# Optimization experiments

Measured on AMD Instinct MI355X. Metric: run time of the kernel, lower is better.

## Reference

```python
import jax, jax.numpy as jnp
import numpy as np

HEADS = 4
HEAD_DIM = 32
NEG_SLOPE = 0.2  # PyG GATConv default

N_NODES = 100000
N_EDGES = 1600000
IN_CH = 128
N_GRAPHS = 64


def setup_inputs() -> dict:
    key = jax.random.key(0)
    ks = jax.random.split(key, 6)
    x = jax.random.normal(ks[0], (N_NODES, IN_CH), dtype=jnp.float32)
    edge_index = jax.random.randint(ks[1], (2, N_EDGES), 0, N_NODES, dtype=jnp.int32)
    batch = jnp.sort(jax.random.randint(ks[2], (N_NODES,), 0, N_GRAPHS, dtype=jnp.int32))
    # glorot-style scaling
    W = jax.random.normal(ks[3], (IN_CH, HEADS * HEAD_DIM), dtype=jnp.float32) * (1.0 / np.sqrt(IN_CH))
    att_src = jax.random.normal(ks[4], (HEADS, HEAD_DIM), dtype=jnp.float32) * (1.0 / np.sqrt(HEAD_DIM))
    att_dst = jax.random.normal(ks[5], (HEADS, HEAD_DIM), dtype=jnp.float32) * (1.0 / np.sqrt(HEAD_DIM))
    bias = jnp.zeros((HEADS * HEAD_DIM,), dtype=jnp.float32)
    return {"x": x, "edge_index": edge_index, "batch": batch,
            "W": W, "att_src": att_src, "att_dst": att_dst, "bias": bias}


def reference(x, edge_index, batch, W, att_src, att_dst, bias):
    # batch is unused (collect_embeddings=False path); kept for signature fidelity
    N = x.shape[0]
    # add self-loops (PyG GATConv default add_self_loops=True)
    loop = jnp.arange(N, dtype=edge_index.dtype)
    src = jnp.concatenate([edge_index[0], loop])  # [E+N]
    dst = jnp.concatenate([edge_index[1], loop])  # [E+N]

    # linear transform, split heads: [N, H, C]
    xt = (x @ W).reshape(N, HEADS, HEAD_DIM)
    a_src = jnp.einsum('nhc,hc->nh', xt, att_src)  # [N, H]
    a_dst = jnp.einsum('nhc,hc->nh', xt, att_dst)  # [N, H]

    # edge-wise attention logits with LeakyReLU
    alpha = a_src[src] + a_dst[dst]                # [E+N, H]
    alpha = jnp.where(alpha >= 0, alpha, NEG_SLOPE * alpha)

    # segment softmax over incoming edges of each destination node
    seg_max = jax.ops.segment_max(alpha, dst, num_segments=N)   # [N, H]
    alpha = jnp.exp(alpha - seg_max[dst])
    seg_sum = jax.ops.segment_sum(alpha, dst, num_segments=N)   # [N, H]
    alpha = alpha / (seg_sum[dst] + 1e-16)

    # weighted scatter-aggregate of source features
    msg = xt[src] * alpha[:, :, None]                            # [E+N, H, C]
    out = jax.ops.segment_sum(msg, dst, num_segments=N)          # [N, H, C]
    out = out.reshape(N, HEADS * HEAD_DIM) + bias                # concat heads
    return jax.nn.relu(out)
```

## Files before the change

### kernel.cpp

```cpp
#include <hip/hip_runtime.h>
#include <hip/hip_bf16.h>

#define HEADS 4
#define CH 128
#define NTILE 9
#define NCOLS (NTILE*16)
#define WSTRIDE 136
#define CAP 64

typedef __attribute__((ext_vector_type(8))) short short8v;
typedef __attribute__((ext_vector_type(4))) float f32x4;

static __device__ __forceinline__ unsigned short f2bf(float f) {
    __hip_bfloat16 b = __float2bfloat16(f);
    return *reinterpret_cast<unsigned short*>(&b);
}
static __device__ __forceinline__ float bf2f(unsigned short u) {
    unsigned int x = ((unsigned int)u) << 16;
    return __uint_as_float(x);
}

__global__ __launch_bounds__(256) void k_prep(
    const float* __restrict__ W, const float* __restrict__ att_src,
    const float* __restrict__ att_dst, unsigned short* __restrict__ Wt)
{
    int idx = blockIdx.x * 256 + threadIdx.x;
    if (idx >= NCOLS * WSTRIDE) return;
    int c = idx / WSTRIDE;
    int k = idx % WSTRIDE;
    float v = 0.f;
    if (k < CH) {
        if (c < CH) {
            v = W[(size_t)k * CH + c];
        } else if (c < CH + 8) {
            int q = c - CH;
            const float* att = (q < 4) ? att_src : att_dst;
            int h = q & 3;
            float s = 0.f;
            #pragma unroll
            for (int t = 0; t < 32; ++t)
                s += W[(size_t)k * CH + h * 32 + t] * att[h * 32 + t];
            v = s;
        }
    }
    Wt[idx] = f2bf(v);
}

__global__ __launch_bounds__(256, 4) void k_fused(
    const float* __restrict__ x, const unsigned short* __restrict__ Wt,
    unsigned short* __restrict__ xt, float* __restrict__ a_src, float* __restrict__ a_dst,
    int N, const int* __restrict__ ei, int E,
    int* __restrict__ cursor, int* __restrict__ csr, int gemmBlocks, int scatB)
{
    __shared__ unsigned short Wl[NCOLS * WSTRIDE];
    const int tid = threadIdx.x;

    if ((int)blockIdx.x >= gemmBlocks) {
        int b     = blockIdx.x - gemmBlocks;
        int slice = b & 7;
        int c     = b >> 3;
        int B     = scatB >> 3;
        int lo = (int)((long long)N * slice / 8);
        int hi = (int)((long long)N * (slice + 1) / 8);
        for (int i = c * 256 + tid; i < E; i += B * 256) {
            int dst = ei[E + i];
            if (dst >= lo && dst < hi) {
                int pos = atomicAdd(&cursor[dst], 1);
                if (pos < CAP) csr[((size_t)dst << 6) + pos] = ei[i];
            }
        }
        return;
    }

    {
        const float4* s4 = (const float4*)Wt;
        float4* d4 = (float4*)Wl;
        for (int i = tid; i < NCOLS * WSTRIDE * 2 / 16; i += 256)
            d4[i] = s4[i];
    }
    __syncthreads();

    const int wv = tid >> 6;
    const int l  = tid & 63;
    const int la = l & 15;
    const int lb = l >> 4;

    const int r = blockIdx.x * 64 + wv * 16 + la;

    float4 f[4][2];
    if (r < N) {
        const float4* p = (const float4*)(x + (size_t)r * CH);
        #pragma unroll
        for (int ks = 0; ks < 4; ++ks) {
            f[ks][0] = p[ks * 8 + lb * 2];
            f[ks][1] = p[ks * 8 + lb * 2 + 1];
        }
    } else {
        #pragma unroll
        for (int ks = 0; ks < 4; ++ks)
            f[ks][0] = f[ks][1] = make_float4(0.f, 0.f, 0.f, 0.f);
    }

    union U8 { short8v v; unsigned short u[8]; };
    short8v a[4];
    #pragma unroll
    for (int ks = 0; ks < 4; ++ks) {
        U8 ua;
        ua.u[0] = f2bf(f[ks][0].x); ua.u[1] = f2bf(f[ks][0].y);
        ua.u[2] = f2bf(f[ks][0].z); ua.u[3] = f2bf(f[ks][0].w);
        ua.u[4] = f2bf(f[ks][1].x); ua.u[5] = f2bf(f[ks][1].y);
        ua.u[6] = f2bf(f[ks][1].z); ua.u[7] = f2bf(f[ks][1].w);
        a[ks] = ua.v;
    }

    f32x4 acc[NTILE];
    #pragma unroll
    for (int n = 0; n < NTILE; ++n) acc[n] = (f32x4){0.f, 0.f, 0.f, 0.f};

    #pragma unroll
    for (int ks = 0; ks < 4; ++ks) {
        #pragma unroll
        for (int n = 0; n < NTILE; ++n) {
            short8v b = *(const short8v*)&Wl[(n * 16 + la) * WSTRIDE + ks * 32 + lb * 8];
            acc[n] = __builtin_amdgcn_mfma_f32_16x16x32_bf16(a[ks], b, acc[n], 0, 0, 0);
        }
    }

    const int rbase = blockIdx.x * 64 + wv * 16 + lb * 4;
    #pragma unroll
    for (int reg = 0; reg < 4; ++reg) {
        int gr = rbase + reg;
        if (gr >= N) continue;
        #pragma unroll
        for (int n = 0; n < 8; ++n)
            xt[(size_t)gr * CH + n * 16 + la] = f2bf(acc[n][reg]);
        if (la < 4)       a_src[(size_t)gr * 4 + la]       = acc[8][reg];
        else if (la < 8)  a_dst[(size_t)gr * 4 + (la - 4)] = acc[8][reg];
    }
}

__global__ __launch_bounds__(256) void k_gather(
    const int* __restrict__ cursor, const int* __restrict__ csr,
    const float* __restrict__ a_src, const float* __restrict__ a_dst,
    const unsigned short* __restrict__ xt, const float* __restrict__ bias,
    float* __restrict__ out, int N)
{
    int n = blockIdx.x * 4 + (threadIdx.x >> 6);
    if (n >= N) return;
    int l   = threadIdx.x & 63;
    int grp = l >> 4;
    int q   = l & 15;
    int h   = q >> 2;

    float ad = a_dst[(size_t)n * 4 + h];
    int cnt = cursor[n];
    if (cnt > CAP) cnt = CAP;
    const size_t base = (size_t)n << 6;

    float acc[8] = {0.f,0.f,0.f,0.f,0.f,0.f,0.f,0.f};
    float wsum = 0.f;
    for (int k = grp; k < cnt; k += 4) {
        int src = csr[base + k];
        float as = a_src[(size_t)src * 4 + h];
        float lg = as + ad;
        lg = (lg >= 0.f) ? lg : 0.2f * lg;
        float w = __expf(lg);
        wsum += w;
        float4 raw = ((const float4*)xt)[(size_t)src * 16 + q];
        union { float4 f; unsigned short u[8]; } uu; uu.f = raw;
        #pragma unroll
        for (int j = 0; j < 8; ++j) acc[j] += w * bf2f(uu.u[j]);
    }
    if (grp == 0) {
        float as = a_src[(size_t)n * 4 + h];
        float lg = as + ad;
        lg = (lg >= 0.f) ? lg : 0.2f * lg;
        float w = __expf(lg);
        wsum += w;
        float4 raw = ((const float4*)xt)[(size_t)n * 16 + q];
        union { float4 f; unsigned short u[8]; } uu; uu.f = raw;
        #pragma unroll
        for (int j = 0; j < 8; ++j) acc[j] += w * bf2f(uu.u[j]);
    }

    #pragma unroll
    for (int j = 0; j < 8; ++j) {
        acc[j] += __shfl_xor(acc[j], 16, 64);
        acc[j] += __shfl_xor(acc[j], 32, 64);
    }
    wsum += __shfl_xor(wsum, 16, 64);
    wsum += __shfl_xor(wsum, 32, 64);

    if (grp == 0) {
        float inv = 1.0f / wsum;
        float4 b0 = ((const float4*)bias)[q * 2];
        float4 b1 = ((const float4*)bias)[q * 2 + 1];
        float4 v0, v1;
        v0.x = fmaxf(fmaf(acc[0], inv, b0.x), 0.f);
        v0.y = fmaxf(fmaf(acc[1], inv, b0.y), 0.f);
        v0.z = fmaxf(fmaf(acc[2], inv, b0.z), 0.f);
        v0.w = fmaxf(fmaf(acc[3], inv, b0.w), 0.f);
        v1.x = fmaxf(fmaf(acc[4], inv, b1.x), 0.f);
        v1.y = fmaxf(fmaf(acc[5], inv, b1.y), 0.f);
        v1.z = fmaxf(fmaf(acc[6], inv, b1.z), 0.f);
        v1.w = fmaxf(fmaf(acc[7], inv, b1.w), 0.f);
        ((float4*)out)[(size_t)n * 32 + q * 2]     = v0;
        ((float4*)out)[(size_t)n * 32 + q * 2 + 1] = v1;
    }
}

extern "C" void kernel_launch(void* const* d_in, const int* in_sizes, int n_in,
                              void* d_out, int out_size, void* d_ws, size_t ws_size,
                              hipStream_t stream) {
    const float* x       = (const float*)d_in[0];
    const int*   ei      = (const int*)d_in[1];
    const float* W       = (const float*)d_in[3];
    const float* att_src = (const float*)d_in[4];
    const float* att_dst = (const float*)d_in[5];
    const float* bias    = (const float*)d_in[6];

    const int N = in_sizes[0] / CH;
    const int E = in_sizes[1] / 2;
    float* out = (float*)d_out;

    char* ws = (char*)d_ws;
    size_t p = 0;
    unsigned short* Wt = (unsigned short*)(ws + p); p += (size_t)NCOLS * WSTRIDE * 2;
    unsigned short* xt = (unsigned short*)(ws + p); p += (size_t)N * CH * 2;
    float* a_src  = (float*)(ws + p); p += (size_t)N * 4 * 4;
    float* a_dst  = (float*)(ws + p); p += (size_t)N * 4 * 4;
    int*   cursor = (int*)(ws + p);   p += (size_t)N * 4;
    int*   csr    = (int*)(ws + p);   p += (size_t)N * CAP * 4;

    hipMemsetAsync(cursor, 0, (size_t)N * 4, stream);

    k_prep<<<(NCOLS * WSTRIDE + 255) / 256, 256, 0, stream>>>(W, att_src, att_dst, Wt);

    const int gemmBlocks = (N + 63) / 64;
    const int scatB      = 1024;
    k_fused<<<gemmBlocks + scatB, 256, 0, stream>>>(x, Wt, xt, a_src, a_dst,
                                                    N, ei, E, cursor, csr,
                                                    gemmBlocks, scatB);

    k_gather<<<(N + 3) / 4, 256, 0, stream>>>(cursor, csr, a_src, a_dst,
                                              xt, bias, out, N);
}
```

Measured before the change: 181.5 us.

## Split fused scatter/GEMM kernel; stage x through swizzled LDS and coalesce xt stores

Separates the CSR scatter and the GEMM into two kernels, so the scatter no longer shares a launch with the GEMM and now runs 2048 blocks instead of 1024. The GEMM no longer copies the weight matrix into LDS; it reads B fragments directly from global memory, which is small enough to be served from cache. It loads and converts x into a swizzled LDS tile with coalesced reads, and stages the output through LDS so xt is written as full-row float4 stores instead of scattered 2-byte stores. This gives up concurrent execution of the two phases and relies on cache hits for the weight reads, in exchange for lower LDS use and higher occupancy.

```diff
diff --git a/kernel.cpp b/kernel.cpp
--- a/kernel.cpp
+++ b/kernel.cpp
@@ -46,37 +46,31 @@
     Wt[idx] = f2bf(v);
 }
 
-__global__ __launch_bounds__(256, 4) void k_fused(
+__global__ __launch_bounds__(256, 6) void k_gemm(
     const float* __restrict__ x, const unsigned short* __restrict__ Wt,
     unsigned short* __restrict__ xt, float* __restrict__ a_src, float* __restrict__ a_dst,
-    int N, const int* __restrict__ ei, int E,
-    int* __restrict__ cursor, int* __restrict__ csr, int gemmBlocks, int scatB)
-{
-    __shared__ unsigned short Wl[NCOLS * WSTRIDE];
+    int N)
+{
+    __shared__ unsigned short xl[64 * CH];
+    char* xb = (char*)xl;
     const int tid = threadIdx.x;
-
-    if ((int)blockIdx.x >= gemmBlocks) {
-        int b     = blockIdx.x - gemmBlocks;
-        int slice = b & 7;
-        int c     = b >> 3;
-        int B     = scatB >> 3;
-        int lo = (int)((long long)N * slice / 8);
-        int hi = (int)((long long)N * (slice + 1) / 8);
-        for (int i = c * 256 + tid; i < E; i += B * 256) {
-            int dst = ei[E + i];
-            if (dst >= lo && dst < hi) {
-                int pos = atomicAdd(&cursor[dst], 1);
-                if (pos < CAP) csr[((size_t)dst << 6) + pos] = ei[i];
-            }
-        }
-        return;
-    }
+    const int blk = blockIdx.x;
 
     {
-        const float4* s4 = (const float4*)Wt;
-        float4* d4 = (float4*)Wl;
-        for (int i = tid; i < NCOLS * WSTRIDE * 2 / 16; i += 256)
-            d4[i] = s4[i];
+        const float4* x4 = (const float4*)x;
+        #pragma unroll
+        for (int it = 0; it < 8; ++it) {
+            int i   = tid + it * 256;
+            int row = i >> 5, c4 = i & 31;
+            int gr  = blk * 64 + row;
+            float4 v = make_float4(0.f, 0.f, 0.f, 0.f);
+            if (gr < N) v = x4[(size_t)gr * 32 + c4];
+            ushort4 u;
+            u.x = f2bf(v.x); u.y = f2bf(v.y); u.z = f2bf(v.z); u.w = f2bf(v.w);
+            int byte = (row << 8) + (c4 << 3);
+            byte ^= (row & 15) << 4;
+            *(ushort4*)(xb + byte) = u;
+        }
     }
     __syncthreads();
 
@@ -84,34 +78,16 @@
     const int l  = tid & 63;
     const int la = l & 15;
     const int lb = l >> 4;
-
-    const int r = blockIdx.x * 64 + wv * 16 + la;
-
-    float4 f[4][2];
-    if (r < N) {
-        const float4* p = (const float4*)(x + (size_t)r * CH);
-        #pragma unroll
-        for (int ks = 0; ks < 4; ++ks) {
-            f[ks][0] = p[ks * 8 + lb * 2];
-            f[ks][1] = p[ks * 8 + lb * 2 + 1];
-        }
-    } else {
-        #pragma unroll
-        for (int ks = 0; ks < 4; ++ks)
-            f[ks][0] = f[ks][1] = make_float4(0.f, 0.f, 0.f, 0.f);
-    }
-
-    union U8 { short8v v; unsigned short u[8]; };
+    const int row = wv * 16 + la;
+
     short8v a[4];
     #pragma unroll
     for (int ks = 0; ks < 4; ++ks) {
-        U8 ua;
-        ua.u[0] = f2bf(f[ks][0].x); ua.u[1] = f2bf(f[ks][0].y);
-        ua.u[2] = f2bf(f[ks][0].z); ua.u[3] = f2bf(f[ks][0].w);
-        ua.u[4] = f2bf(f[ks][1].x); ua.u[5] = f2bf(f[ks][1].y);
-        ua.u[6] = f2bf(f[ks][1].z); ua.u[7] = f2bf(f[ks][1].w);
-        a[ks] = ua.v;
-    }
+        int byte = (row << 8) + (ks << 6) + (lb << 4);
+        byte ^= la << 4;
+        a[ks] = *(const short8v*)(xb + byte);
+    }
+    __syncthreads();
 
     f32x4 acc[NTILE];
     #pragma unroll
@@ -121,21 +97,67 @@
     for (int ks = 0; ks < 4; ++ks) {
         #pragma unroll
         for (int n = 0; n < NTILE; ++n) {
-            short8v b = *(const short8v*)&Wl[(n * 16 + la) * WSTRIDE + ks * 32 + lb * 8];
-            acc[n] = __builtin_amdgcn_mfma_f32_16x16x32_bf16(a[ks], b, acc[n], 0, 0, 0);
-        }
-    }
-
-    const int rbase = blockIdx.x * 64 + wv * 16 + lb * 4;
+            short8v bb = *(const short8v*)&Wt[(size_t)(n * 16 + la) * WSTRIDE + ks * 32 + lb * 8];
+            acc[n] = __builtin_amdgcn_mfma_f32_16x16x32_bf16(a[ks], bb, acc[n], 0, 0, 0);
+        }
+    }
+
     #pragma unroll
     for (int reg = 0; reg < 4; ++reg) {
-        int gr = rbase + reg;
-        if (gr >= N) continue;
-        #pragma unroll
-        for (int n = 0; n < 8; ++n)
-            xt[(size_t)gr * CH + n * 16 + la] = f2bf(acc[n][reg]);
-        if (la < 4)       a_src[(size_t)gr * 4 + la]       = acc[8][reg];
-        else if (la < 8)  a_dst[(size_t)gr * 4 + (la - 4)] = acc[8][reg];
+        int r = wv * 16 + lb * 4 + reg;
+        int swz = (r & 15) << 4;
+        #pragma unroll
+        for (int n = 0; n < 8; ++n) {
+            int byte = (r << 8) + ((n * 16 + la) << 1);
+            *(unsigned short*)(xb + (byte ^ swz)) = f2bf(acc[n][reg]);
+        }
+    }
+    __syncthreads();
+
+    {
+        #pragma unroll
+        for (int it = 0; it < 4; ++it) {
+            int j   = tid + it * 256;
+            int r   = j >> 4, g = j & 15;
+            int gr  = blk * 64 + r;
+            if (gr < N) {
+                int byte = (r << 8) + (g << 4);
+                byte ^= (r & 15) << 4;
+                float4 v = *(const float4*)(xb + byte);
+                ((float4*)xt)[(size_t)gr * 16 + g] = v;
+            }
+        }
+    }
+
+    {
+        int rbase = blk * 64 + wv * 16 + lb * 4;
+        #pragma unroll
+        for (int reg = 0; reg < 4; ++reg) {
+            int gr = rbase + reg;
+            if (gr < N) {
+                if (la < 4)       a_src[(size_t)gr * 4 + la]       = acc[8][reg];
+                else if (la < 8)  a_dst[(size_t)gr * 4 + (la - 4)] = acc[8][reg];
+            }
+        }
+    }
+}
+
+__global__ __launch_bounds__(256) void k_scatter(
+    const int* __restrict__ ei, int E, int N,
+    int* __restrict__ cursor, int* __restrict__ csr)
+{
+    int slice = blockIdx.x & 7;
+    int c     = blockIdx.x >> 3;
+    int B     = gridDim.x >> 3;
+    int lo = (int)((long long)N * slice / 8);
+    int hi = (int)((long long)N * (slice + 1) / 8);
+
+    for (int i = c * 256 + threadIdx.x; i < E; i += B * 256) {
+        int dst = ei[E + i];
+        if (dst >= lo && dst < hi) {
+            int pos = atomicAdd(&cursor[dst], 1);
+            if (pos < CAP) csr[((size_t)dst << 6) + pos] = ei[i];
+        }
     }
 }
 
@@ -236,11 +258,9 @@
 
     k_prep<<<(NCOLS * WSTRIDE + 255) / 256, 256, 0, stream>>>(W, att_src, att_dst, Wt);
 
-    const int gemmBlocks = (N + 63) / 64;
-    const int scatB      = 1024;
-    k_fused<<<gemmBlocks + scatB, 256, 0, stream>>>(x, Wt, xt, a_src, a_dst,
-                                                    N, ei, E, cursor, csr,
-                                                    gemmBlocks, scatB);
+    k_scatter<<<2048, 256, 0, stream>>>(ei, E, N, cursor, csr);
+
+    k_gemm<<<(N + 63) / 64, 256, 0, stream>>>(x, Wt, xt, a_src, a_dst, N);
 
     k_gather<<<(N + 3) / 4, 256, 0, stream>>>(cursor, csr, a_src, a_dst,
                                               xt, bias, out, N);
```

After: 191.8 us. 1.06x slower.
